# Performance work log

Hardware: AMD Instinct MI355X
Metric: run time of the kernel (lower is better)

## Reference

```python
import jax, jax.numpy as jnp
import numpy as np

B = 16384       # batch
F = 40          # total fields
ND = 13         # dense fields (Linear(1 -> E))
NS = 27         # sparse fields (Embedding(V, E))
E = 16          # embedding size
V = 100000      # vocab per categorical field
D0 = F * E      # 640, deep input dim
H1, H2 = 512, 256
EPS = 1e-5


def setup_inputs() -> dict:
    key = jax.random.key(0)
    ks = jax.random.split(key, 16)
    s = 0.05
    Xi = jax.random.randint(ks[0], (B, F, 1), 0, V)                 # int64 indices; first 13 used as float values
    Xv = jax.random.uniform(ks[1], (B, F), dtype=jnp.float32)       # per-field value multipliers
    bias = jax.random.normal(ks[2], (B,), dtype=jnp.float32)        # the torch code makes a fresh randn bias per call
    # first-order params: 13 Linear(1->E) + 27 Embedding(V,E)
    dw1 = jax.random.normal(ks[3], (ND, E), dtype=jnp.float32) * s  # Linear weights [13,E] (in_features=1)
    db1 = jax.random.normal(ks[4], (ND, E), dtype=jnp.float32) * s
    e1 = jax.random.normal(ks[5], (NS, V, E), dtype=jnp.float32) * s
    # second-order params (separate set, same structure)
    dw2 = jax.random.normal(ks[6], (ND, E), dtype=jnp.float32) * s
    db2 = jax.random.normal(ks[7], (ND, E), dtype=jnp.float32) * s
    e2 = jax.random.normal(ks[8], (NS, V, E), dtype=jnp.float32) * s
    # deep MLP: 640 -> 512 -> 256 with batchnorm (loop only builds linear_1, linear_2)
    W1 = jax.random.normal(ks[9], (D0, H1), dtype=jnp.float32) * s
    b1 = jnp.zeros((H1,), dtype=jnp.float32)
    g1 = jnp.ones((H1,), dtype=jnp.float32)
    bt1 = jnp.zeros((H1,), dtype=jnp.float32)
    W2 = jax.random.normal(ks[10], (H1, H2), dtype=jnp.float32) * s
    b2 = jnp.zeros((H2,), dtype=jnp.float32)
    g2 = jnp.ones((H2,), dtype=jnp.float32)
    bt2 = jnp.zeros((H2,), dtype=jnp.float32)
    return dict(Xi=Xi, Xv=Xv, bias=bias, dw1=dw1, db1=db1, e1=e1,
                dw2=dw2, db2=db2, e2=e2,
                W1=W1, b1=b1, g1=g1, bt1=bt1, W2=W2, b2=b2, g2=g2, bt2=bt2)


def _field_embed(Xi, Xv, dw, db, emb):
    # dense fields: Linear(1->E) on the scalar value Xi[:, i, 0]
    x_dense = Xi[:, :ND, 0].astype(jnp.float32)                     # [B,13]
    dense = x_dense[:, :, None] * dw[None] + db[None]               # [B,13,E]
    # sparse fields: embedding gather (sum over length-1 bag == identity)
    idx = Xi[:, ND:, 0]                                             # [B,27]
    sparse = emb[jnp.arange(NS)[None, :], idx]                      # [B,27,E]
    e = jnp.concatenate([dense, sparse], axis=1)                    # [B,40,E]
    return e * Xv[:, :, None]                                       # per-field scale by Xv


def _batchnorm(x, g, b):
    mu = x.mean(0)
    var = x.var(0)  # biased, matches torch BN training normalization
    return (x - mu) * jax.lax.rsqrt(var + EPS) * g + b


def reference(Xi, Xv, bias, dw1, db1, e1, dw2, db2, e2,
              W1, b1, g1, bt1, W2, b2, g2, bt2):
    fo = _field_embed(Xi, Xv, dw1, db1, e1)                         # [B,40,E]
    fm_first = fo.reshape(B, -1)                                    # [B,640]
    so = _field_embed(Xi, Xv, dw2, db2, e2)                         # [B,40,E]
    s = so.sum(axis=1)                                              # [B,E]
    fm_second = 0.5 * (s * s - (so * so).sum(axis=1))               # [B,E]
    deep = so.reshape(B, -1)                                        # [B,640]
    deep = _batchnorm(deep @ W1 + b1, g1, bt1)
    deep = _batchnorm(deep @ W2 + b2, g2, bt2)
    # dropout is identity here (deterministic reference)
    return fm_first.sum(axis=1) + fm_second.sum(axis=1) + deep.sum(axis=1) + bias
```

## Files before the change

### kernel.cpp

```cpp
#include <hip/hip_runtime.h>


#define B_ROWS 16384
#define VOCAB 100000
#define D0 640
#define H1 512
#define H2 256
#define EPSV 1e-5f

typedef short bf16x8 __attribute__((ext_vector_type(8)));
typedef float f32x4 __attribute__((ext_vector_type(4)));
typedef unsigned short u16;

struct Params {
    const int* Xi; const float* Xv; const float* bias;
    const float* dw1; const float* db1; const float* e1;
    const float* dw2; const float* db2; const float* e2;
    const float* W1; const float* g1; const float* bt1;
    const float* W2; const float* g2; const float* bt2;
    u16* so_bf; float* partial; u16* W1T; u16* W2T;
    float* psum1; float* psq1; float* psum2; float* psq2;
    float* a1; float* a2; float* c2;
    u16* Z1bf; u16* Z2bf; float* out;
};

__device__ inline u16 f2bf(float x) {
    unsigned u = __float_as_uint(x);
    return (u16)((u + 0x7fffu + ((u >> 16) & 1u)) >> 16);
}
__device__ inline float bf2f(unsigned b) {
    return __uint_as_float((b & 0xffffu) << 16);
}
__device__ inline void async16(const void* g, void* l) {
    __builtin_amdgcn_global_load_lds(
        (const __attribute__((address_space(1))) void*)g,
        (__attribute__((address_space(3))) void*)l, 16, 0, 0);
}

__global__ __launch_bounds__(256) void embed_prep_k(Params p) {
    __shared__ float tile[32][33];
    __shared__ u16 so_lds[16][648];
    __shared__ __align__(16) int   xi_lds[16][40];
    __shared__ __align__(16) float xv_lds[16][40];
    __shared__ __align__(16) float w_lds[4][208];
    const int bid = blockIdx.x, tid = threadIdx.x;
    const int rblk = (bid & 7) * 128 + (bid >> 3);

    if (tid < 160) {
        ((uint4*)&xi_lds[0][0])[tid] = ((const uint4*)(p.Xi + (size_t)rblk * 16 * 40))[tid];
        ((uint4*)&xv_lds[0][0])[tid] = ((const uint4*)(p.Xv + (size_t)rblk * 16 * 40))[tid];
    }
    if (tid < 52)        ((uint4*)&w_lds[0][0])[tid]       = ((const uint4*)p.dw1)[tid];
    else if (tid < 104)  ((uint4*)&w_lds[1][0])[tid - 52]  = ((const uint4*)p.db1)[tid - 52];
    else if (tid < 156)  ((uint4*)&w_lds[2][0])[tid - 104] = ((const uint4*)p.dw2)[tid - 104];
    else if (tid < 208)  ((uint4*)&w_lds[3][0])[tid - 156] = ((const uint4*)p.db2)[tid - 156];

    if (bid < 448) {
        const float* W; u16* WT; int K, N, k0, n0;
        if (bid < 320) { W = p.W1; WT = p.W1T; K = D0; N = H1; k0 = (bid % 20) * 32; n0 = (bid / 20) * 32; }
        else { int b2 = bid - 320; W = p.W2; WT = p.W2T; K = H1; N = H2; k0 = (b2 % 16) * 32; n0 = (b2 / 16) * 32; }
        int tx = tid & 31, ty4 = (tid >> 5) * 4;
#pragma unroll
        for (int r = 0; r < 4; ++r)
            tile[ty4 + r][tx] = W[(size_t)(k0 + ty4 + r) * N + n0 + tx];
        __syncthreads();
#pragma unroll
        for (int r = 0; r < 4; ++r)
            WT[(size_t)(n0 + ty4 + r) * K + k0 + tx] = f2bf(tile[tx][ty4 + r]);
    }
    __syncthreads();

    const int e = tid & 15;
    const int r = tid >> 4;
    const int b = rblk * 16 + r;

    float accf = 0.f, s1 = 0.f, sq = 0.f;
#pragma unroll
    for (int f = 0; f < 13; ++f) {
        float x = (float)xi_lds[r][f];
        float xv = xv_lds[r][f];
        float fo = (x * w_lds[0][f * 16 + e] + w_lds[1][f * 16 + e]) * xv;
        float so = (x * w_lds[2][f * 16 + e] + w_lds[3][f * 16 + e]) * xv;
        accf += fo; s1 += so; sq += so * so;
        so_lds[r][f * 16 + e] = f2bf(so);
    }
#pragma unroll 1
    for (int c = 0; c < 3; ++c) {
        const int base = 13 + c * 9;
        int   ix[9]; float xv9[9], v1[9], v2[9];
#pragma unroll
        for (int s = 0; s < 9; ++s) { ix[s] = xi_lds[r][base + s]; xv9[s] = xv_lds[r][base + s]; }
#pragma unroll
        for (int s = 0; s < 9; ++s) {
            size_t off = (size_t)(base - 13 + s) * (VOCAB * 16) + (size_t)ix[s] * 16 + e;
            v1[s] = p.e1[off];
            v2[s] = p.e2[off];
        }
#pragma unroll
        for (int s = 0; s < 9; ++s) {
            float fo = v1[s] * xv9[s], so = v2[s] * xv9[s];
            accf += fo; s1 += so; sq += so * so;
            so_lds[r][(base + s) * 16 + e] = f2bf(so);
        }
    }
    float val = accf + 0.5f * (s1 * s1 - sq);
    val += __shfl_xor(val, 1); val += __shfl_xor(val, 2);
    val += __shfl_xor(val, 4); val += __shfl_xor(val, 8);
    if (e == 0) p.partial[b] = val + p.bias[b];

    __syncthreads();
    uint4* gdst = (uint4*)(p.so_bf + (size_t)rblk * 16 * D0);
#pragma unroll
    for (int k = 0; k < 5; ++k) {
        int v = k * 256 + tid;
        int row = v / 80, c16 = v - row * 80;
        gdst[v] = *(const uint4*)&so_lds[row][c16 * 8];
    }
}

__global__ __launch_bounds__(256) void gemm1_k(Params p) {
    __shared__ u16 As[3][128 * 32];
    __shared__ u16 Bs[3][128 * 32];
    const int tid = threadIdx.x, lane = tid & 63, w = tid >> 6;
    const int bid = (int)blockIdx.x;
    const int g = bid >> 3, x = bid & 7;
    const int mt = x * 16 + (g >> 2), nt = g & 3;
    const int m0 = mt * 128, n0 = nt * 128;
    const int wr = w >> 1, wc = w & 1;

    f32x4 acc[4][4] = {};

    auto stage = [&](int buf, int kt) {
#pragma unroll
        for (int j = 0; j < 2; ++j) {
            int s = j * 256 + tid;
            int row = s >> 2;
            int c8 = ((s ^ (s >> 3)) & 3) * 8;
            async16(p.so_bf + (size_t)(m0 + row) * D0 + kt + c8,
                    &As[buf][(j * 256 + w * 64) * 8]);
            async16(p.W1T + (size_t)(n0 + row) * D0 + kt + c8,
                    &Bs[buf][(j * 256 + w * 64) * 8]);
        }
    };

    const int NT = D0 / 32;
    stage(0, 0);
    stage(1, 32);
    for (int t = 0; t < NT; ++t) {
        if (t < NT - 1) asm volatile("s_waitcnt vmcnt(4)" ::: "memory");
        else            asm volatile("s_waitcnt vmcnt(0)" ::: "memory");
        __builtin_amdgcn_s_barrier();
        __builtin_amdgcn_sched_barrier(0);
        if (t + 2 < NT) stage((t + 2) % 3, (t + 2) * 32);
        const u16* Ac = As[t % 3];
        const u16* Bc = Bs[t % 3];
        const int gq = lane >> 4;
        bf16x8 af[4], bfr[4];
#pragma unroll
        for (int i = 0; i < 4; ++i) {
            int ar = wr * 64 + i * 16 + (lane & 15);
            af[i] = *(const bf16x8*)&Ac[ar * 32 + ((gq ^ ((ar >> 1) & 3)) * 8)];
            int br = wc * 64 + i * 16 + (lane & 15);
            bfr[i] = *(const bf16x8*)&Bc[br * 32 + ((gq ^ ((br >> 1) & 3)) * 8)];
        }
#pragma unroll
        for (int i = 0; i < 4; ++i)
#pragma unroll
            for (int j2 = 0; j2 < 4; ++j2)
                acc[i][j2] = __builtin_amdgcn_mfma_f32_16x16x32_bf16(
                    af[i], bfr[j2], acc[i][j2], 0, 0, 0);
    }
#pragma unroll
    for (int i = 0; i < 4; ++i)
#pragma unroll
        for (int j2 = 0; j2 < 4; ++j2) {
            int row = m0 + wr * 64 + i * 16 + (lane >> 4) * 4;
            int col = n0 + wc * 64 + j2 * 16 + (lane & 15);
#pragma unroll
            for (int q = 0; q < 4; ++q)
                p.Z1bf[(size_t)(row + q) * H1 + col] = f2bf(acc[i][j2][q]);
        }
    const int chunk = mt * 2 + wr;
#pragma unroll
    for (int j2 = 0; j2 < 4; ++j2) {
        float s = 0.f, q = 0.f;
#pragma unroll
        for (int i = 0; i < 4; ++i)
#pragma unroll
            for (int qq = 0; qq < 4; ++qq) { float v = acc[i][j2][qq]; s += v; q += v * v; }
        s += __shfl_xor(s, 16); s += __shfl_xor(s, 32);
        q += __shfl_xor(q, 16); q += __shfl_xor(q, 32);
        if (lane < 16) {
            int col = n0 + wc * 64 + j2 * 16 + lane;
            p.psum1[(size_t)chunk * H1 + col] = s;
            p.psq1[(size_t)chunk * H1 + col] = q;
        }
    }
}

__global__ __launch_bounds__(256) void finstats1_k(Params p) {
    int col = blockIdx.x * 8 + (threadIdx.x >> 5);
    int l32 = threadIdx.x & 31;
    float s = 0.f, q = 0.f;
#pragma unroll
    for (int k = 0; k < 8; ++k) {
        int ch = k * 32 + l32;
        s += p.psum1[(size_t)ch * H1 + col];
        q += p.psq1[(size_t)ch * H1 + col];
    }
#pragma unroll
    for (int m = 1; m <= 16; m <<= 1) {
        s += __shfl_xor(s, m);
        q += __shfl_xor(q, m);
    }
    if (l32 == 0) {
        const float inv = 1.0f / (float)B_ROWS;
        float mean = s * inv;
        float var = q * inv - mean * mean;
        p.a1[col] = p.g1[col] * rsqrtf(var + EPSV);
    }
}

__global__ __launch_bounds__(256) void gemm2_k(Params p) {
    __shared__ u16 As[2][128 * 64];
    __shared__ u16 Bs[2][64 * 64];
    const int tid = threadIdx.x, lane = tid & 63, w = tid >> 6;
    const int bid = (int)blockIdx.x;
    const int g = bid >> 3, x = bid & 7;
    const int mt = x * 16 + (g >> 2), nt = g & 3;
    const int m0 = mt * 128, n0 = nt * 64;
    const int wr = w >> 1, wc = w & 1;
    const int srow = lane >> 3;
    const int scol_sw = ((lane ^ (lane >> 3)) & 7) * 8;

    f32x4 acc[4][2] = {};

    auto stageA = [&](int buf, int kt) {
#pragma unroll
        for (int j = 0; j < 4; ++j) {
            int r0 = w * 32 + j * 8;
            async16(p.Z1bf + (size_t)(m0 + r0 + srow) * H1 + kt + scol_sw,
                    &As[buf][r0 * 64]);
        }
    };
    auto loadB = [&](uint4* br, int kt) {
#pragma unroll
        for (int r = 0; r < 2; ++r) {
            int li = r * 256 + tid, row = li >> 3, c8 = (li & 7) * 8;
            br[r] = *(const uint4*)(p.W2T + (size_t)(n0 + row) * H1 + kt + c8);
        }
    };
    auto writeB = [&](int buf, const uint4* br, int kt) {
#pragma unroll
        for (int r = 0; r < 2; ++r) {
            int li = r * 256 + tid, row = li >> 3, c8 = (li & 7) * 8;
            float4 alo = *(const float4*)(p.a1 + kt + c8);
            float4 ahi = *(const float4*)(p.a1 + kt + c8 + 4);
            uint4 z = br[r];
            uint4 o;
            o.x = (unsigned)f2bf(bf2f(z.x) * alo.x) | ((unsigned)f2bf(bf2f(z.x >> 16) * alo.y) << 16);
            o.y = (unsigned)f2bf(bf2f(z.y) * alo.z) | ((unsigned)f2bf(bf2f(z.y >> 16) * alo.w) << 16);
            o.z = (unsigned)f2bf(bf2f(z.z) * ahi.x) | ((unsigned)f2bf(bf2f(z.z >> 16) * ahi.y) << 16);
            o.w = (unsigned)f2bf(bf2f(z.w) * ahi.z) | ((unsigned)f2bf(bf2f(z.w >> 16) * ahi.w) << 16);
            int csw = ((li ^ (li >> 3)) & 7) * 8;
            *(uint4*)&Bs[buf][row * 64 + csw] = o;
        }
    };

    uint4 breg[2];
    stageA(0, 0);
    loadB(breg, 0);
    writeB(0, breg, 0);
    __syncthreads();
    int cur = 0;
    for (int t = 0; t < 8; ++t) {
        uint4 bnx[2];
        if (t < 7) { stageA(cur ^ 1, (t + 1) * 64); loadB(bnx, (t + 1) * 64); }
#pragma unroll
        for (int kk = 0; kk < 2; ++kk) {
            bf16x8 af[4], bfr[2];
#pragma unroll
            for (int i = 0; i < 4; ++i) {
                int ar = wr * 64 + i * 16 + (lane & 15);
                int gq = kk * 4 + (lane >> 4);
                af[i] = *(const bf16x8*)&As[cur][ar * 64 + ((gq ^ (ar & 7)) * 8)];
            }
#pragma unroll
            for (int j2 = 0; j2 < 2; ++j2) {
                int br = wc * 32 + j2 * 16 + (lane & 15);
                int gq = kk * 4 + (lane >> 4);
                bfr[j2] = *(const bf16x8*)&Bs[cur][br * 64 + ((gq ^ (br & 7)) * 8)];
            }
#pragma unroll
            for (int i = 0; i < 4; ++i)
#pragma unroll
                for (int j2 = 0; j2 < 2; ++j2)
                    acc[i][j2] = __builtin_amdgcn_mfma_f32_16x16x32_bf16(
                        af[i], bfr[j2], acc[i][j2], 0, 0, 0);
        }
        if (t < 7) writeB(cur ^ 1, bnx, (t + 1) * 64);
        __syncthreads();
        cur ^= 1;
    }
#pragma unroll
    for (int i = 0; i < 4; ++i)
#pragma unroll
        for (int j2 = 0; j2 < 2; ++j2) {
            int row = m0 + wr * 64 + i * 16 + (lane >> 4) * 4;
            int col = n0 + wc * 32 + j2 * 16 + (lane & 15);
#pragma unroll
            for (int q = 0; q < 4; ++q)
                p.Z2bf[(size_t)(row + q) * H2 + col] = f2bf(acc[i][j2][q]);
        }
    const int chunk = mt * 2 + wr;
#pragma unroll
    for (int j2 = 0; j2 < 2; ++j2) {
        float s = 0.f, q = 0.f;
#pragma unroll
        for (int i = 0; i < 4; ++i)
#pragma unroll
            for (int qq = 0; qq < 4; ++qq) { float v = acc[i][j2][qq]; s += v; q += v * v; }
        s += __shfl_xor(s, 16); s += __shfl_xor(s, 32);
        q += __shfl_xor(q, 16); q += __shfl_xor(q, 32);
        if (lane < 16) {
            int col = n0 + wc * 32 + j2 * 16 + lane;
            p.psum2[(size_t)chunk * H2 + col] = s;
            p.psq2[(size_t)chunk * H2 + col] = q;
        }
    }
}

__global__ __launch_bounds__(256) void finstats2_k(Params p) {
    int col = blockIdx.x * 8 + (threadIdx.x >> 5);
    int l32 = threadIdx.x & 31;
    float s = 0.f, q = 0.f;
#pragma unroll
    for (int k = 0; k < 8; ++k) {
        int ch = k * 32 + l32;
        s += p.psum2[(size_t)ch * H2 + col];
        q += p.psq2[(size_t)ch * H2 + col];
    }
#pragma unroll
    for (int m = 1; m <= 16; m <<= 1) {
        s += __shfl_xor(s, m);
        q += __shfl_xor(q, m);
    }
    if (l32 == 0) {
        const float inv = 1.0f / (float)B_ROWS;
        float mean = s * inv;
        float var = q * inv - mean * mean;
        float av = p.g2[col] * rsqrtf(var + EPSV);
        p.a2[col] = av;
        p.c2[col] = p.bt2[col] - mean * av;
    }
}

__global__ __launch_bounds__(256) void final_k(Params p) {
    int w = threadIdx.x >> 6, lane = threadIdx.x & 63;
    int j = (int)blockIdx.x;
    int gblk = (j & 7) * 512 + (j >> 3);
    int b = gblk * 4 + w;
    ushort4 z4 = *(const ushort4*)(p.Z2bf + (size_t)b * H2 + lane * 4);
    float4 a = *(const float4*)(p.a2 + lane * 4);
    float4 c = *(const float4*)(p.c2 + lane * 4);
    float v = bf2f(z4.x) * a.x + c.x + bf2f(z4.y) * a.y + c.y
            + bf2f(z4.z) * a.z + c.z + bf2f(z4.w) * a.w + c.w;
#pragma unroll
    for (int m = 1; m < 64; m <<= 1) v += __shfl_xor(v, m);
    if (lane == 0) p.out[b] = p.partial[b] + v;
}

extern "C" void kernel_launch(void* const* d_in, const int* in_sizes, int n_in,
                              void* d_out, int out_size, void* d_ws, size_t ws_size,
                              hipStream_t stream)
{
    Params p;
    p.Xi   = (const int*)d_in[0];
    p.Xv   = (const float*)d_in[1];
    p.bias = (const float*)d_in[2];
    p.dw1  = (const float*)d_in[3];
    p.db1  = (const float*)d_in[4];
    p.e1   = (const float*)d_in[5];
    p.dw2  = (const float*)d_in[6];
    p.db2  = (const float*)d_in[7];
    p.e2   = (const float*)d_in[8];
    p.W1   = (const float*)d_in[9];
    p.g1   = (const float*)d_in[11];
    p.bt1  = (const float*)d_in[12];
    p.W2   = (const float*)d_in[13];
    p.g2   = (const float*)d_in[15];
    p.bt2  = (const float*)d_in[16];

    char* ws = (char*)d_ws;
    size_t off = 0;
    auto alloc = [&](size_t bytes) { char* q = ws + off; off += (bytes + 255) & ~(size_t)255; return q; };
    p.so_bf   = (u16*)alloc((size_t)B_ROWS * D0 * 2);
    p.partial = (float*)alloc((size_t)B_ROWS * 4);
    p.W1T     = (u16*)alloc((size_t)H1 * D0 * 2);
    p.W2T     = (u16*)alloc((size_t)H2 * H1 * 2);
    p.psum1   = (float*)alloc((size_t)256 * H1 * 4);
    p.psq1    = (float*)alloc((size_t)256 * H1 * 4);
    p.psum2   = (float*)alloc((size_t)256 * H2 * 4);
    p.psq2    = (float*)alloc((size_t)256 * H2 * 4);
    p.a1      = (float*)alloc(H1 * 4);
    p.a2      = (float*)alloc(H2 * 4);
    p.c2      = (float*)alloc(H2 * 4);
    p.Z1bf    = (u16*)alloc((size_t)B_ROWS * H1 * 2);
    p.Z2bf    = (u16*)alloc((size_t)B_ROWS * H2 * 2);
    p.out     = (float*)d_out;
    (void)in_sizes; (void)n_in; (void)out_size; (void)ws_size;

    embed_prep_k<<<1024, 256, 0, stream>>>(p);
    gemm1_k    <<<512, 256, 0, stream>>>(p);
    finstats1_k<<<64, 256, 0, stream>>>(p);
    gemm2_k    <<<512, 256, 0, stream>>>(p);
    finstats2_k<<<32, 256, 0, stream>>>(p);
    final_k    <<<B_ROWS / 4, 256, 0, stream>>>(p);
}
```

Before: 73.73 us.

## Deepen GEMM pipelines to 4 stages and prescale W2 in finstats

gemm1 moves from a 3-buffer to a 4-buffer LDS ring, so three K-tiles are in flight. finstats1 now folds the BN scale a1 into a bf16 copy of W2 (W2s). This lets gemm2 drop its register load, scale and store path for B and stream both operands with async global-to-LDS loads in a 4-stage, 32-wide K pipeline. The change costs extra LDS per block, which may lower occupancy, plus an extra scaled-weight buffer written by the small stats kernel.

Result: slower. 76.41 us (+3.6%).

```diff
diff --git a/kernel.cpp b/kernel.cpp
--- a/kernel.cpp
+++ b/kernel.cpp
@@ -18,7 +18,7 @@
     const float* dw2; const float* db2; const float* e2;
     const float* W1; const float* g1; const float* bt1;
     const float* W2; const float* g2; const float* bt2;
-    u16* so_bf; float* partial; u16* W1T; u16* W2T;
+    u16* so_bf; float* partial; u16* W1T; u16* W2T; u16* W2s;
     float* psum1; float* psq1; float* psum2; float* psq2;
     float* a1; float* a2; float* c2;
     u16* Z1bf; u16* Z2bf; float* out;
@@ -119,8 +119,8 @@
 }
 
 __global__ __launch_bounds__(256) void gemm1_k(Params p) {
-    __shared__ u16 As[3][128 * 32];
-    __shared__ u16 Bs[3][128 * 32];
+    __shared__ u16 As[4][128 * 32];
+    __shared__ u16 Bs[4][128 * 32];
     const int tid = threadIdx.x, lane = tid & 63, w = tid >> 6;
     const int bid = (int)blockIdx.x;
     const int g = bid >> 3, x = bid & 7;
@@ -146,14 +146,16 @@
     const int NT = D0 / 32;
     stage(0, 0);
     stage(1, 32);
+    stage(2, 64);
     for (int t = 0; t < NT; ++t) {
-        if (t < NT - 1) asm volatile("s_waitcnt vmcnt(4)" ::: "memory");
-        else            asm volatile("s_waitcnt vmcnt(0)" ::: "memory");
+        if (t < NT - 2)       asm volatile("s_waitcnt vmcnt(8)" ::: "memory");
+        else if (t == NT - 2) asm volatile("s_waitcnt vmcnt(4)" ::: "memory");
+        else                  asm volatile("s_waitcnt vmcnt(0)" ::: "memory");
         __builtin_amdgcn_s_barrier();
         __builtin_amdgcn_sched_barrier(0);
-        if (t + 2 < NT) stage((t + 2) % 3, (t + 2) * 32);
-        const u16* Ac = As[t % 3];
-        const u16* Bc = Bs[t % 3];
+        if (t + 3 < NT) stage((t + 3) & 3, (t + 3) * 32);
+        const u16* Ac = As[t & 3];
+        const u16* Bc = Bs[t & 3];
         const int gq = lane >> 4;
         bf16x8 af[4], bfr[4];
 #pragma unroll
@@ -213,94 +215,79 @@
         s += __shfl_xor(s, m);
         q += __shfl_xor(q, m);
     }
-    if (l32 == 0) {
-        const float inv = 1.0f / (float)B_ROWS;
-        float mean = s * inv;
-        float var = q * inv - mean * mean;
-        p.a1[col] = p.g1[col] * rsqrtf(var + EPSV);
+    const float inv = 1.0f / (float)B_ROWS;
+    float mean = s * inv;
+    float var = q * inv - mean * mean;
+    float av = p.g1[col] * rsqrtf(var + EPSV);
+    if (l32 == 0) p.a1[col] = av;
+#pragma unroll
+    for (int k = 0; k < 8; ++k) {
+        int n = k * 32 + l32;
+        p.W2s[(size_t)n * H1 + col] = f2bf(bf2f(p.W2T[(size_t)n * H1 + col]) * av);
     }
 }
 
 __global__ __launch_bounds__(256) void gemm2_k(Params p) {
-    __shared__ u16 As[2][128 * 64];
-    __shared__ u16 Bs[2][64 * 64];
+    __shared__ u16 As[4][128 * 32];
+    __shared__ u16 Bs[4][64 * 32];
     const int tid = threadIdx.x, lane = tid & 63, w = tid >> 6;
     const int bid = (int)blockIdx.x;
     const int g = bid >> 3, x = bid & 7;
     const int mt = x * 16 + (g >> 2), nt = g & 3;
     const int m0 = mt * 128, n0 = nt * 64;
     const int wr = w >> 1, wc = w & 1;
-    const int srow = lane >> 3;
-    const int scol_sw = ((lane ^ (lane >> 3)) & 7) * 8;
 
     f32x4 acc[4][2] = {};
 
-    auto stageA = [&](int buf, int kt) {
-#pragma unroll
-        for (int j = 0; j < 4; ++j) {
-            int r0 = w * 32 + j * 8;
-            async16(p.Z1bf + (size_t)(m0 + r0 + srow) * H1 + kt + scol_sw,
-                    &As[buf][r0 * 64]);
+    auto stage = [&](int buf, int kt) {
+#pragma unroll
+        for (int j = 0; j < 2; ++j) {
+            int s = j * 256 + tid;
+            int row = s >> 2;
+            int c8 = ((s ^ (s >> 3)) & 3) * 8;
+            async16(p.Z1bf + (size_t)(m0 + row) * H1 + kt + c8,
+                    &As[buf][(j * 256 + w * 64) * 8]);
+        }
+        {
+            int s = tid;
+            int row = s >> 2;
+            int c8 = ((s ^ (s >> 3)) & 3) * 8;
+            async16(p.W2s + (size_t)(n0 + row) * H1 + kt + c8,
+                    &Bs[buf][(w * 64) * 8]);
         }
     };
-    auto loadB = [&](uint4* br, int kt) {
-#pragma unroll
-        for (int r = 0; r < 2; ++r) {
-            int li = r * 256 + tid, row = li >> 3, c8 = (li & 7) * 8;
-            br[r] = *(const uint4*)(p.W2T + (size_t)(n0 + row) * H1 + kt + c8);
-        }
-    };
-    auto writeB = [&](int buf, const uint4* br, int kt) {
-#pragma unroll
-        for (int r = 0; r < 2; ++r) {
-            int li = r * 256 + tid, row = li >> 3, c8 = (li & 7) * 8;
-            float4 alo = *(const float4*)(p.a1 + kt + c8);
-            float4 ahi = *(const float4*)(p.a1 + kt + c8 + 4);
-            uint4 z = br[r];
-            uint4 o;
-            o.x = (unsigned)f2bf(bf2f(z.x) * alo.x) | ((unsigned)f2bf(bf2f(z.x >> 16) * alo.y) << 16);
-            o.y = (unsigned)f2bf(bf2f(z.y) * alo.z) | ((unsigned)f2bf(bf2f(z.y >> 16) * alo.w) << 16);
-            o.z = (unsigned)f2bf(bf2f(z.z) * ahi.x) | ((unsigned)f2bf(bf2f(z.z >> 16) * ahi.y) << 16);
-            o.w = (unsigned)f2bf(bf2f(z.w) * ahi.z) | ((unsigned)f2bf(bf2f(z.w >> 16) * ahi.w) << 16);
-            int csw = ((li ^ (li >> 3)) & 7) * 8;
-            *(uint4*)&Bs[buf][row * 64 + csw] = o;
-        }
-    };
-
-    uint4 breg[2];
-    stageA(0, 0);
-    loadB(breg, 0);
-    writeB(0, breg, 0);
-    __syncthreads();
-    int cur = 0;
-    for (int t = 0; t < 8; ++t) {
-        uint4 bnx[2];
-        if (t < 7) { stageA(cur ^ 1, (t + 1) * 64); loadB(bnx, (t + 1) * 64); }
-#pragma unroll
-        for (int kk = 0; kk < 2; ++kk) {
-            bf16x8 af[4], bfr[2];
-#pragma unroll
-            for (int i = 0; i < 4; ++i) {
-                int ar = wr * 64 + i * 16 + (lane & 15);
-                int gq = kk * 4 + (lane >> 4);
-                af[i] = *(const bf16x8*)&As[cur][ar * 64 + ((gq ^ (ar & 7)) * 8)];
-            }
-#pragma unroll
-            for (int j2 = 0; j2 < 2; ++j2) {
-                int br = wc * 32 + j2 * 16 + (lane & 15);
-                int gq = kk * 4 + (lane >> 4);
-                bfr[j2] = *(const bf16x8*)&Bs[cur][br * 64 + ((gq ^ (br & 7)) * 8)];
-            }
-#pragma unroll
-            for (int i = 0; i < 4; ++i)
-#pragma unroll
-                for (int j2 = 0; j2 < 2; ++j2)
-                    acc[i][j2] = __builtin_amdgcn_mfma_f32_16x16x32_bf16(
-                        af[i], bfr[j2], acc[i][j2], 0, 0, 0);
-        }
-        if (t < 7) writeB(cur ^ 1, bnx, (t + 1) * 64);
-        __syncthreads();
-        cur ^= 1;
+
+    const int NT = H1 / 32;
+    stage(0, 0);
+    stage(1, 32);
+    stage(2, 64);
+    for (int t = 0; t < NT; ++t) {
+        if (t < NT - 2)       asm volatile("s_waitcnt vmcnt(6)" ::: "memory");
+        else if (t == NT - 2) asm volatile("s_waitcnt vmcnt(3)" ::: "memory");
+        else                  asm volatile("s_waitcnt vmcnt(0)" ::: "memory");
+        __builtin_amdgcn_s_barrier();
+        __builtin_amdgcn_sched_barrier(0);
+        if (t + 3 < NT) stage((t + 3) & 3, (t + 3) * 32);
+        const u16* Ac = As[t & 3];
+        const u16* Bc = Bs[t & 3];
+        const int gq = lane >> 4;
+        bf16x8 af[4], bfr[2];
+#pragma unroll
+        for (int i = 0; i < 4; ++i) {
+            int ar = wr * 64 + i * 16 + (lane & 15);
+            af[i] = *(const bf16x8*)&Ac[ar * 32 + ((gq ^ ((ar >> 1) & 3)) * 8)];
+        }
+#pragma unroll
+        for (int j2 = 0; j2 < 2; ++j2) {
+            int br = wc * 32 + j2 * 16 + (lane & 15);
+            bfr[j2] = *(const bf16x8*)&Bc[br * 32 + ((gq ^ ((br >> 1) & 3)) * 8)];
+        }
+#pragma unroll
+        for (int i = 0; i < 4; ++i)
+#pragma unroll
+            for (int j2 = 0; j2 < 2; ++j2)
+                acc[i][j2] = __builtin_amdgcn_mfma_f32_16x16x32_bf16(
+                    af[i], bfr[j2], acc[i][j2], 0, 0, 0);
     }
 #pragma unroll
     for (int i = 0; i < 4; ++i)
@@ -398,6 +385,7 @@
     p.partial = (float*)alloc((size_t)B_ROWS * 4);
     p.W1T     = (u16*)alloc((size_t)H1 * D0 * 2);
     p.W2T     = (u16*)alloc((size_t)H2 * H1 * 2);
+    p.W2s     = (u16*)alloc((size_t)H2 * H1 * 2);
     p.psum1   = (float*)alloc((size_t)256 * H1 * 4);
     p.psq1    = (float*)alloc((size_t)256 * H1 * 4);
     p.psum2   = (float*)alloc((size_t)256 * H2 * 4);
```
